# Kernel tuning notes

Measured on AMD Instinct MI355X. Metric: run time of the kernel, lower is better.

The kernel has to match this reference:

```python
import jax, jax.numpy as jnp
import numpy as np

NUM_ATOMS = 24
HID = 61          # embedding width before extended features
H = HID + 3       # conv/GRU width (degree+cycle+charge)
EMB = 64
NUM_CG = 18
NUM_ITERS = 6


def setup_inputs() -> dict:
    key = jax.random.key(0)
    ks = jax.random.split(key, 24)
    N, E = 20000, 60000
    s = 0.05
    p = lambda k, shp: (jax.random.normal(k, shp, dtype=jnp.float32) * s)
    return {
        "x": jax.random.randint(ks[0], (N, 1), 0, NUM_ATOMS),
        "edge_index": jax.random.randint(ks[1], (2, E), 0, N),
        "edge_attr": jax.random.uniform(ks[2], (E, 4), dtype=jnp.float32),
        "extended_feat": jax.random.normal(ks[3], (N, 3), dtype=jnp.float32),
        # nn.Embedding(input_dim, hidden_dim)
        "embed": p(ks[4], (NUM_ATOMS, HID)),
        # edge_nn: Linear(4,128) -> ReLU -> Linear(128, H*H)
        "We1": p(ks[5], (4, 128)), "be1": p(ks[6], (128,)),
        "We2": p(ks[7], (128, H * H)), "be2": p(ks[8], (H * H,)),
        # NNConv root weight + bias
        "root": p(ks[9], (H, H)), "conv_b": p(ks[10], (H,)),
        # GRU(H, H): torch layout [3H, H] gates order (r, z, n)
        "Wih": p(ks[11], (3 * H, H)), "Whh": p(ks[12], (3 * H, H)),
        "bih": p(ks[13], (3 * H,)), "bhh": p(ks[14], (3 * H,)),
        # output_fc: Linear(H,H) -> ReLU -> Linear(H, EMB)
        "Wo1": p(ks[15], (H, H)), "bo1": p(ks[16], (H,)),
        "Wo2": p(ks[17], (H, EMB)), "bo2": p(ks[18], (EMB,)),
        # cg_type_fc: Linear(EMB+NUM_ATOMS+3, 256) -> ReLU -> Linear(256, 18)
        "Wc1": p(ks[19], (EMB + NUM_ATOMS + 3, 256)), "bc1": p(ks[20], (256,)),
        "Wc2": p(ks[21], (256, NUM_CG)), "bc2": p(ks[22], (NUM_CG,)),
    }


def reference(x, edge_index, edge_attr, extended_feat, embed,
              We1, be1, We2, be2, root, conv_b,
              Wih, Whh, bih, bhh, Wo1, bo1, Wo2, bo2,
              Wc1, bc1, Wc2, bc2):
    N = x.shape[0]
    E = edge_index.shape[1]
    idx = x[:, 0]
    src, dst = edge_index[0], edge_index[1]

    # input_fc + relu, concat extended features -> [N, H]
    out = jax.nn.relu(embed[idx])
    out = jnp.concatenate([out, extended_feat], axis=1)
    h = out

    # edge_nn: per-edge [H, H] weight (edge_attr is constant across iterations)
    W_edge = (jax.nn.relu(edge_attr @ We1 + be1) @ We2 + be2).reshape(E, H, H)

    for _ in range(NUM_ITERS):
        # NNConv: gather source feats, per-edge matmul, scatter-add to targets
        msg = jnp.einsum('eh,ehk->ek', out[src], W_edge)          # [E, H]
        agg = jax.ops.segment_sum(msg, dst, num_segments=N)       # [N, H]
        m = jax.nn.relu(agg + out @ root + conv_b)
        # GRU cell (torch gate order r, z, n)
        gi = m @ Wih.T + bih
        gh = h @ Whh.T + bhh
        r = jax.nn.sigmoid(gi[:, :H] + gh[:, :H])
        z = jax.nn.sigmoid(gi[:, H:2 * H] + gh[:, H:2 * H])
        n = jnp.tanh(gi[:, 2 * H:] + r * gh[:, 2 * H:])
        h = (1.0 - z) * n + z * h
        out = h

    # output_fc
    out = jax.nn.relu(out @ Wo1 + bo1) @ Wo2 + bo2                # [N, EMB]

    atom_onehot = jax.nn.one_hot(idx, NUM_ATOMS, dtype=out.dtype)
    feat = jnp.concatenate([out, atom_onehot, extended_feat], axis=1)
    fg_embed = feat / jnp.maximum(
        jnp.linalg.norm(feat, axis=1, keepdims=True), 1e-12)
    node_cg_type_pred = jax.nn.relu(fg_embed @ Wc1 + bc1) @ Wc2 + bc2
    return fg_embed, node_cg_type_pred
```

## Files before the change

### kernel.cpp

```cpp
#include <hip/hip_runtime.h>
#include <hip/hip_fp16.h>

#define NATOMS 24
#define HIDD   61
#define NITERS 6
#define CTOT   132
#define HC     66

typedef unsigned short u16;
typedef unsigned int   u32;
typedef _Float16 f16x8 __attribute__((ext_vector_type(8)));
typedef float    f32x4 __attribute__((ext_vector_type(4)));

#define GLOAD_LDS16(g, l) __builtin_amdgcn_global_load_lds( \
    (const __attribute__((address_space(1))) void*)(g), \
    (__attribute__((address_space(3))) void*)(l), 16, 0, 0)

__device__ __forceinline__ float sigm(float x){ return 1.f/(1.f + __expf(-x)); }
__device__ __forceinline__ float tanhx(float x){ return 1.f - 2.f/(__expf(2.f*x)+1.f); }
__device__ __forceinline__ u16 f2h(float f){ return __half_as_ushort(__float2half(f)); }
__device__ __forceinline__ float hbits2f(u16 b){
  union { u16 u; __half h; } cv; cv.u = b; return __half2float(cv.h);
}

__device__ __forceinline__ f16x8 vmul8(f16x8 v, _Float16 s){
  f16x8 r;
  #pragma unroll
  for (int i=0;i<8;++i) r[i] = v[i]*s;
  return r;
}

__global__ void k_init_h(const int* __restrict__ x, const float* __restrict__ embed,
                         const float* __restrict__ ext, float* __restrict__ h, int N){
  int t = blockIdx.x*blockDim.x + threadIdx.x;
  if (t >= N*64) return;
  int n = t >> 6, k = t & 63;
  float v;
  if (k < HIDD) v = fmaxf(embed[x[n]*HIDD + k], 0.f);
  else          v = ext[n*3 + (k - HIDD)];
  h[t] = v;
}

__global__ void k_prep_B(const float* __restrict__ We2, const float* __restrict__ be2,
                         u16* __restrict__ Bg){
  int tid = blockIdx.x*blockDim.x + threadIdx.x;
  if (tid >= CTOT*8*64) return;
  int l  = tid & 63;
  int fi = tid >> 6;
  int ct = fi & 3;
  int kh = (fi >> 2) & 1;
  int c  = fi >> 3;
  int n  = ct*16 + (l & 15);
  int hb = kh*32 + (l >> 4)*8;
  u16 ov[8];
  #pragma unroll
  for (int j=0;j<8;++j){
    int hh = hb + j;
    float v = 0.f;
    if (c < 128)       v = We2[(size_t)c*4096 + hh*64 + n];
    else if (c == 128) v = be2[hh*64 + n];
    ov[j] = f2h(v);
  }
  uint4 o;
  o.x = (u32)ov[0] | ((u32)ov[1]<<16);
  o.y = (u32)ov[2] | ((u32)ov[3]<<16);
  o.z = (u32)ov[4] | ((u32)ov[5]<<16);
  o.w = (u32)ov[6] | ((u32)ov[7]<<16);
  *(uint4*)&Bg[(size_t)fi*512 + l*8] = o;
}

__global__ void k_prep_W(const float* __restrict__ Wo1, const float* __restrict__ Wo2,
                         const float* __restrict__ Wc1, const float* __restrict__ Wc2,
                         u16* __restrict__ Wf){
  int tid = blockIdx.x*blockDim.x + threadIdx.x;
  if (tid >= 80*64) return;
  int l  = tid & 63;
  int fi = tid >> 6;
  int lr = l & 15, lq = l >> 4;
  u16 ov[8];
  #pragma unroll
  for (int j=0;j<8;++j){
    float v = 0.f;
    if (fi < 8){
      int ct = fi >> 1, kh = fi & 1;
      int n = ct*16 + lr, k = kh*32 + lq*8 + j;
      v = Wo1[k*64 + n];
    } else if (fi < 16){
      int f2 = fi - 8;
      int ct = f2 >> 1, kh = f2 & 1;
      int n = ct*16 + lr, k = kh*32 + lq*8 + j;
      v = Wo2[k*64 + n];
    } else if (fi < 64){
      int f2 = fi - 16;
      int cti = f2 / 3, kh = f2 % 3;
      int n = cti*16 + lr, k = kh*32 + lq*8 + j;
      if (k < 91) v = Wc1[k*256 + n];
    } else {
      int f2 = fi - 64;
      int kh = f2 >> 1, ct = f2 & 1;
      int n = ct*16 + lr, k = kh*32 + lq*8 + j;
      if (n < 18) v = Wc2[k*18 + n];
    }
    ov[j] = f2h(v);
  }
  uint4 o;
  o.x = (u32)ov[0] | ((u32)ov[1]<<16);
  o.y = (u32)ov[2] | ((u32)ov[3]<<16);
  o.z = (u32)ov[4] | ((u32)ov[5]<<16);
  o.w = (u32)ov[6] | ((u32)ov[7]<<16);
  *(uint4*)&Wf[(size_t)fi*512 + l*8] = o;
}

__global__ void k_prep_C(const float* __restrict__ root, const float* __restrict__ Wih,
                         const float* __restrict__ Whh, u16* __restrict__ Cf){
  int tid = blockIdx.x*blockDim.x + threadIdx.x;
  if (tid >= 56*64) return;
  int l  = tid & 63;
  int fi = tid >> 6;
  int lr = l & 15, lq = l >> 4;
  u16 ov[8];
  #pragma unroll
  for (int j=0;j<8;++j){
    float v;
    int k = (fi < 8 ? (fi & 1) : ((fi - 8) & 1)) * 32 + lq*8 + j;
    if (fi < 8){
      int ct = fi >> 1;
      v = root[k*64 + ct*16 + lr];
    } else if (fi < 32){
      int cti = (fi - 8) >> 1;
      v = Wih[(cti*16 + lr)*64 + k];
    } else {
      int cti = (fi - 32) >> 1;
      v = Whh[(cti*16 + lr)*64 + k];
    }
    ov[j] = f2h(v);
  }
  uint4 o;
  o.x = (u32)ov[0] | ((u32)ov[1]<<16);
  o.y = (u32)ov[2] | ((u32)ov[3]<<16);
  o.z = (u32)ov[4] | ((u32)ov[5]<<16);
  o.w = (u32)ov[6] | ((u32)ov[7]<<16);
  *(uint4*)&Cf[(size_t)fi*512 + l*8] = o;
}

__global__ __launch_bounds__(256) void k_edge_mlp(
    const float* __restrict__ ea, const float* __restrict__ We1,
    const float* __restrict__ be1, u16* __restrict__ AgT, int E, int Epad)
{
  __shared__ float Al[128][66];
  int t = threadIdx.x;
  int e0 = blockIdx.x * 64;
  int el = t & 63, cg = t >> 6;
  int e = e0 + el;
  float4 av = make_float4(0,0,0,0);
  if (e < E) av = *(const float4*)&ea[(size_t)e*4];
  for (int cc = 0; cc < 32; ++cc){
    int c = cg*32 + cc;
    float v = be1[c] + av.x*We1[c] + av.y*We1[128+c] + av.z*We1[256+c] + av.w*We1[384+c];
    Al[c][el] = fmaxf(v, 0.f);
  }
  __syncthreads();
  for (int idx = t; idx < 64*33; idx += 256){
    int el2 = idx / 33, q = idx % 33;
    u16 ov[4];
    #pragma unroll
    for (int i=0;i<4;++i){
      int c = q*4 + i;
      float v;
      if (c < 128)       v = Al[c][el2];
      else if (c == 128) v = 1.f;
      else               v = 0.f;
      ov[i] = f2h(v);
    }
    ushort4 o; o.x=ov[0]; o.y=ov[1]; o.z=ov[2]; o.w=ov[3];
    *(ushort4*)&AgT[(size_t)(e0+el2)*CTOT + q*4] = o;
  }
}

__global__ __launch_bounds__(512,4) void k_msg_mfma(
    const int* __restrict__ ei, const float* __restrict__ h,
    const u16* __restrict__ AgT, const u16* __restrict__ Bg,
    float* __restrict__ agg, int E, int Epad)
{
  __shared__ __align__(16) u16 Blds[2][2][8192];
  __shared__ int dstl[128];
  int t = threadIdx.x;
  int lane = t & 63;
  int w = t >> 6;
  int eg = w & 3;
  int half = w >> 2;
  int e0 = blockIdx.x * 128;
  int slot0 = half * HC;

  if (t < 128) dstl[t] = (e0 + t < E) ? ei[E + e0 + t] : -1;

  f16x8 vf[2][2];
  #pragma unroll
  for (int rt=0; rt<2; ++rt){
    int e = e0 + eg*32 + rt*16 + (lane&15);
    int src = (e < E) ? ei[e] : 0;
    const float* hp = &h[(size_t)src*64 + (lane>>4)*8];
    #pragma unroll
    for (int kh=0; kh<2; ++kh){
      float4 a = *(const float4*)&hp[kh*32];
      float4 b = *(const float4*)&hp[kh*32+4];
      f16x8 v;
      v[0]=(_Float16)a.x; v[1]=(_Float16)a.y; v[2]=(_Float16)a.z; v[3]=(_Float16)a.w;
      v[4]=(_Float16)b.x; v[5]=(_Float16)b.y; v[6]=(_Float16)b.z; v[7]=(_Float16)b.w;
      vf[rt][kh] = v;
    }
  }

  f32x4 acc[2][4];
  #pragma unroll
  for (int i=0;i<2;++i)
    #pragma unroll
    for (int j=0;j<4;++j)
      acc[i][j] = (f32x4){0.f,0.f,0.f,0.f};

  const u16* Ae[2];
  #pragma unroll
  for (int rt=0; rt<2; ++rt)
    Ae[rt] = AgT + (size_t)(e0 + eg*32 + rt*16 + (lane&15))*CTOT + slot0;

  union UA { ushort2 u; _Float16 hv[2]; };
  _Float16 arP[2][2], arN[2][2];
  #pragma unroll
  for (int rt=0;rt<2;++rt){
    UA ua; ua.u = *(const ushort2*)&Ae[rt][0];
    arP[rt][0] = ua.hv[0]; arP[rt][1] = ua.hv[1];
  }

  {
    const char* g = (const char*)(Bg + (size_t)slot0*4096);
    #pragma unroll
    for (int r=0;r<4;++r)
      GLOAD_LDS16(g + r*4096 + eg*1024 + lane*16,
                  (char*)&Blds[half][0][0] + r*4096 + eg*1024);
  }
  __syncthreads();

  int cur = 0;
  for (int ci = 0; ci < 33; ++ci){
    if (ci + 1 < 33){
      const char* g = (const char*)(Bg + (size_t)(slot0 + (ci+1)*2)*4096);
      #pragma unroll
      for (int r=0;r<4;++r)
        GLOAD_LDS16(g + r*4096 + eg*1024 + lane*16,
                    (char*)&Blds[half][cur^1][0] + r*4096 + eg*1024);
      #pragma unroll
      for (int rt=0;rt<2;++rt){
        UA ua; ua.u = *(const ushort2*)&Ae[rt][(ci+1)*2];
        arN[rt][0] = ua.hv[0]; arN[rt][1] = ua.hv[1];
      }
    }
    const u16* Bb = &Blds[half][cur][0];
    #pragma unroll
    for (int cl=0; cl<2; ++cl){
      #pragma unroll
      for (int kh=0; kh<2; ++kh){
        f16x8 g0 = vmul8(vf[0][kh], arP[0][cl]);
        f16x8 g1 = vmul8(vf[1][kh], arP[1][cl]);
        #pragma unroll
        for (int ct=0; ct<4; ++ct){
          f16x8 bf = *(const f16x8*)&Bb[(cl*8 + kh*4 + ct)*512 + lane*8];
          acc[0][ct] = __builtin_amdgcn_mfma_f32_16x16x32_f16(g0, bf, acc[0][ct], 0,0,0);
          acc[1][ct] = __builtin_amdgcn_mfma_f32_16x16x32_f16(g1, bf, acc[1][ct], 0,0,0);
        }
      }
    }
    __syncthreads();
    #pragma unroll
    for (int rt=0;rt<2;++rt){ arP[rt][0] = arN[rt][0]; arP[rt][1] = arN[rt][1]; }
    cur ^= 1;
  }

  float* accl = (float*)&Blds[0][0][0];
  if (half == 1){
    #pragma unroll
    for (int rt=0; rt<2; ++rt)
      #pragma unroll
      for (int ct=0; ct<4; ++ct)
        *(f32x4*)&accl[(size_t)(eg*8 + rt*4 + ct)*256 + lane*4] = acc[rt][ct];
  }
  __syncthreads();
  if (half == 0){
    #pragma unroll
    for (int rt=0; rt<2; ++rt)
      #pragma unroll
      for (int ct=0; ct<4; ++ct)
        acc[rt][ct] += *(const f32x4*)&accl[(size_t)(eg*8 + rt*4 + ct)*256 + lane*4];
    #pragma unroll
    for (int rt=0; rt<2; ++rt){
      #pragma unroll
      for (int r=0; r<4; ++r){
        int el = eg*32 + rt*16 + (lane>>4)*4 + r;
        int dv = dstl[el];
        if (dv >= 0){
          #pragma unroll
          for (int ct=0; ct<4; ++ct)
            unsafeAtomicAdd(&agg[(size_t)dv*64 + ct*16 + (lane&15)], acc[rt][ct][r]);
        }
      }
    }
  }
}

__global__ __launch_bounds__(256) void k_combine(
    const float* __restrict__ hcur, float* __restrict__ agg,
    const u16* __restrict__ Cf, const float* __restrict__ convb,
    const float* __restrict__ bih, const float* __restrict__ bhh,
    float* __restrict__ hnext, int N)
{
  __shared__ __align__(16) u16  hn[32][72];
  __shared__ __align__(16) u16  mn[32][72];
  __shared__ float hsf[32][68];
  int t = threadIdx.x;
  int lane = t & 63;
  int w = t >> 6;
  int lr = lane & 15, lq = lane >> 4;
  int n0 = blockIdx.x * 32;

  {
    int node = t >> 3, k8 = (t & 7) * 8;
    int n = n0 + node;
    f16x8 v;
    float4 a = make_float4(0,0,0,0), b = make_float4(0,0,0,0);
    if (n < N){
      a = *(const float4*)&hcur[(size_t)n*64 + k8];
      b = *(const float4*)&hcur[(size_t)n*64 + k8 + 4];
    }
    v[0]=(_Float16)a.x; v[1]=(_Float16)a.y; v[2]=(_Float16)a.z; v[3]=(_Float16)a.w;
    v[4]=(_Float16)b.x; v[5]=(_Float16)b.y; v[6]=(_Float16)b.z; v[7]=(_Float16)b.w;
    *(f16x8*)&hn[node][k8] = v;
    *(float4*)&hsf[node][k8] = a;
    *(float4*)&hsf[node][k8+4] = b;
  }
  __syncthreads();

  {
    f32x4 acc[2];
    acc[0] = (f32x4){0.f,0.f,0.f,0.f}; acc[1] = (f32x4){0.f,0.f,0.f,0.f};
    #pragma unroll
    for (int kh=0; kh<2; ++kh){
      f16x8 bf = *(const f16x8*)&Cf[(size_t)(w*2 + kh)*512 + lane*8];
      #pragma unroll
      for (int rt=0; rt<2; ++rt){
        f16x8 af = *(const f16x8*)&hn[rt*16 + lr][kh*32 + lq*8];
        acc[rt] = __builtin_amdgcn_mfma_f32_16x16x32_f16(af, bf, acc[rt], 0,0,0);
      }
    }
    float cb = convb[w*16 + lr];
    #pragma unroll
    for (int rt=0; rt<2; ++rt){
      #pragma unroll
      for (int r=0; r<4; ++r){
        int node = rt*16 + lq*4 + r;
        int n = n0 + node;
        int col = w*16 + lr;
        float ag = 0.f;
        if (n < N){
          ag = agg[(size_t)n*64 + col];
          agg[(size_t)n*64 + col] = 0.f;
        }
        mn[node][col] = f2h(fmaxf(acc[rt][r] + ag + cb, 0.f));
      }
    }
  }
  __syncthreads();

  f32x4 gi[3][2], gh[3][2];
  #pragma unroll
  for (int s=0;s<3;++s)
    #pragma unroll
    for (int rt=0;rt<2;++rt){
      gi[s][rt] = (f32x4){0.f,0.f,0.f,0.f};
      gh[s][rt] = (f32x4){0.f,0.f,0.f,0.f};
    }
  #pragma unroll
  for (int s=0; s<3; ++s){
    int cti = s*4 + w;
    #pragma unroll
    for (int kh=0; kh<2; ++kh){
      f16x8 bfI = *(const f16x8*)&Cf[(size_t)(8  + cti*2 + kh)*512 + lane*8];
      f16x8 bfH = *(const f16x8*)&Cf[(size_t)(32 + cti*2 + kh)*512 + lane*8];
      #pragma unroll
      for (int rt=0; rt<2; ++rt){
        f16x8 am = *(const f16x8*)&mn[rt*16 + lr][kh*32 + lq*8];
        f16x8 ah = *(const f16x8*)&hn[rt*16 + lr][kh*32 + lq*8];
        gi[s][rt] = __builtin_amdgcn_mfma_f32_16x16x32_f16(am, bfI, gi[s][rt], 0,0,0);
        gh[s][rt] = __builtin_amdgcn_mfma_f32_16x16x32_f16(ah, bfH, gh[s][rt], 0,0,0);
      }
    }
  }

  {
    int j = w*16 + lr;
    float bI0 = bih[j], bI1 = bih[64 + j], bI2 = bih[128 + j];
    float bH0 = bhh[j], bH1 = bhh[64 + j], bH2 = bhh[128 + j];
    #pragma unroll
    for (int rt=0; rt<2; ++rt){
      #pragma unroll
      for (int r=0; r<4; ++r){
        int node = rt*16 + lq*4 + r;
        int n = n0 + node;
        if (n < N){
          float rr = sigm(gi[0][rt][r] + bI0 + gh[0][rt][r] + bH0);
          float zz = sigm(gi[1][rt][r] + bI1 + gh[1][rt][r] + bH1);
          float hold = hsf[node][j];
          float nn = tanhx(gi[2][rt][r] + bI2 + rr*(gh[2][rt][r] + bH2));
          hnext[(size_t)n*64 + j] = (1.f - zz)*nn + zz*hold;
        }
      }
    }
  }
}

__global__ __launch_bounds__(256) void k_final(
    const float* __restrict__ h, const int* __restrict__ x, const float* __restrict__ ext,
    const u16* __restrict__ Wf,
    const float* __restrict__ bo1, const float* __restrict__ bo2,
    const float* __restrict__ bc1, const float* __restrict__ bc2,
    float* __restrict__ fg_out, float* __restrict__ pred_out, int N)
{
  __shared__ __align__(16) u16 fgn[32][104];
  __shared__ __align__(16) u16 t1n[32][264];
  int t = threadIdx.x;
  int lane = t & 63;
  int w = t >> 6;
  int lr = lane & 15, lq = lane >> 4;
  int n0 = blockIdx.x * 32;

  {
    int node = t >> 3, k8 = (t & 7) * 8;
    int n = n0 + node;
    f16x8 v;
    if (n < N){
      float4 a = *(const float4*)&h[(size_t)n*64 + k8];
      float4 b = *(const float4*)&h[(size_t)n*64 + k8 + 4];
      v[0]=(_Float16)a.x; v[1]=(_Float16)a.y; v[2]=(_Float16)a.z; v[3]=(_Float16)a.w;
      v[4]=(_Float16)b.x; v[5]=(_Float16)b.y; v[6]=(_Float16)b.z; v[7]=(_Float16)b.w;
    } else {
      #pragma unroll
      for (int i=0;i<8;++i) v[i] = (_Float16)0.f;
    }
    *(f16x8*)&fgn[node][k8] = v;
    if (t < 160){
      int node2 = t / 5, qd = t % 5;
      *(uint4*)&fgn[node2][64 + qd*8] = make_uint4(0,0,0,0);
    }
  }
  __syncthreads();

  {
    f32x4 acc[2];
    acc[0] = (f32x4){0.f,0.f,0.f,0.f}; acc[1] = (f32x4){0.f,0.f,0.f,0.f};
    #pragma unroll
    for (int kh=0; kh<2; ++kh){
      f16x8 bf = *(const f16x8*)&Wf[(size_t)(w*2 + kh)*512 + lane*8];
      #pragma unroll
      for (int rt=0; rt<2; ++rt){
        f16x8 af = *(const f16x8*)&fgn[rt*16 + lr][kh*32 + lq*8];
        acc[rt] = __builtin_amdgcn_mfma_f32_16x16x32_f16(af, bf, acc[rt], 0,0,0);
      }
    }
    float bv = bo1[w*16 + lr];
    #pragma unroll
    for (int rt=0; rt<2; ++rt)
      #pragma unroll
      for (int r=0; r<4; ++r)
        t1n[rt*16 + lq*4 + r][w*16 + lr] = f2h(fmaxf(acc[rt][r] + bv, 0.f));
  }
  __syncthreads();

  {
    f32x4 acc[2];
    acc[0] = (f32x4){0.f,0.f,0.f,0.f}; acc[1] = (f32x4){0.f,0.f,0.f,0.f};
    #pragma unroll
    for (int kh=0; kh<2; ++kh){
      f16x8 bf = *(const f16x8*)&Wf[(size_t)(8 + w*2 + kh)*512 + lane*8];
      #pragma unroll
      for (int rt=0; rt<2; ++rt){
        f16x8 af = *(const f16x8*)&t1n[rt*16 + lr][kh*32 + lq*8];
        acc[rt] = __builtin_amdgcn_mfma_f32_16x16x32_f16(af, bf, acc[rt], 0,0,0);
      }
    }
    float bv = bo2[w*16 + lr];
    #pragma unroll
    for (int rt=0; rt<2; ++rt)
      #pragma unroll
      for (int r=0; r<4; ++r)
        fgn[rt*16 + lq*4 + r][w*16 + lr] = f2h(acc[rt][r] + bv);
  }
  __syncthreads();

  if (t < 32){
    int ni = t, n = n0 + ni;
    if (n < N){
      int idxn = x[n];
      float e0=ext[n*3], e1=ext[n*3+1], e2=ext[n*3+2];
      float ss = 1.f + e0*e0 + e1*e1 + e2*e2;
      for (int j=0;j<64;++j){ float v = hbits2f(fgn[ni][j]); ss += v*v; }
      float rn = 1.f / fmaxf(sqrtf(ss), 1e-12f);
      for (int j=0;j<64;++j) fgn[ni][j] = f2h(hbits2f(fgn[ni][j])*rn);
      #pragma unroll
      for (int c=0;c<24;++c) fgn[ni][64+c] = (c==idxn) ? f2h(rn) : (u16)0;
      fgn[ni][88] = f2h(e0*rn); fgn[ni][89] = f2h(e1*rn); fgn[ni][90] = f2h(e2*rn);
    }
  }
  __syncthreads();

  for (int idx=t; idx<32*91; idx+=256){
    int ni = idx / 91, c = idx % 91;
    int n = n0 + ni;
    if (n < N) fg_out[(size_t)n*91 + c] = hbits2f(fgn[ni][c]);
  }

  {
    f32x4 acc[2][4];
    #pragma unroll
    for (int i=0;i<2;++i)
      #pragma unroll
      for (int j=0;j<4;++j) acc[i][j] = (f32x4){0.f,0.f,0.f,0.f};
    #pragma unroll
    for (int kh=0; kh<3; ++kh){
      f16x8 af[2];
      #pragma unroll
      for (int rt=0; rt<2; ++rt)
        af[rt] = *(const f16x8*)&fgn[rt*16 + lr][kh*32 + lq*8];
      #pragma unroll
      for (int c4=0; c4<4; ++c4){
        int cti = w*4 + c4;
        f16x8 bf = *(const f16x8*)&Wf[(size_t)(16 + cti*3 + kh)*512 + lane*8];
        #pragma unroll
        for (int rt=0; rt<2; ++rt)
          acc[rt][c4] = __builtin_amdgcn_mfma_f32_16x16x32_f16(af[rt], bf, acc[rt][c4], 0,0,0);
      }
    }
    #pragma unroll
    for (int c4=0; c4<4; ++c4){
      float bv = bc1[w*64 + c4*16 + lr];
      #pragma unroll
      for (int rt=0; rt<2; ++rt)
        #pragma unroll
        for (int r=0; r<4; ++r)
          t1n[rt*16 + lq*4 + r][w*64 + c4*16 + lr] = f2h(fmaxf(acc[rt][c4][r] + bv, 0.f));
    }
  }
  __syncthreads();

  {
    int rt = w >> 1, ct = w & 1;
    f32x4 acc = (f32x4){0.f,0.f,0.f,0.f};
    #pragma unroll
    for (int kh=0; kh<8; ++kh){
      f16x8 af = *(const f16x8*)&t1n[rt*16 + lr][kh*32 + lq*8];
      f16x8 bf = *(const f16x8*)&Wf[(size_t)(64 + kh*2 + ct)*512 + lane*8];
      acc = __builtin_amdgcn_mfma_f32_16x16x32_f16(af, bf, acc, 0,0,0);
    }
    int c = ct*16 + lr;
    if (c < 18){
      float bv = bc2[c];
      #pragma unroll
      for (int r=0; r<4; ++r){
        int n = n0 + rt*16 + lq*4 + r;
        if (n < N) pred_out[(size_t)n*18 + c] = acc[r] + bv;
      }
    }
  }
}

extern "C" void kernel_launch(void* const* d_in, const int* in_sizes, int n_in,
                              void* d_out, int out_size, void* d_ws, size_t ws_size,
                              hipStream_t stream)
{
  const int*   x    = (const int*)d_in[0];
  const int*   ei   = (const int*)d_in[1];
  const float* ea   = (const float*)d_in[2];
  const float* ext  = (const float*)d_in[3];
  const float* embed= (const float*)d_in[4];
  const float* We1  = (const float*)d_in[5];
  const float* be1  = (const float*)d_in[6];
  const float* We2  = (const float*)d_in[7];
  const float* be2  = (const float*)d_in[8];
  const float* root = (const float*)d_in[9];
  const float* convb= (const float*)d_in[10];
  const float* Wih  = (const float*)d_in[11];
  const float* Whh  = (const float*)d_in[12];
  const float* bih  = (const float*)d_in[13];
  const float* bhh  = (const float*)d_in[14];
  const float* Wo1  = (const float*)d_in[15];
  const float* bo1  = (const float*)d_in[16];
  const float* Wo2  = (const float*)d_in[17];
  const float* bo2  = (const float*)d_in[18];
  const float* Wc1  = (const float*)d_in[19];
  const float* bc1  = (const float*)d_in[20];
  const float* Wc2  = (const float*)d_in[21];
  const float* bc2  = (const float*)d_in[22];
  int N = in_sizes[0];
  int E = in_sizes[1] / 2;
  float* out = (float*)d_out;
  float* fg_out = out;
  float* pred_out = out + (size_t)N*91;

  int nblk256 = (E + 255) / 256;
  int Epad = nblk256 * 256;
  int nblk128 = (E + 127) / 128;

  char* w = (char*)d_ws;
  size_t remain = ws_size;
  auto alloc = [&](size_t bytes)->char*{
    size_t rb = (bytes + 255) & ~(size_t)255;
    if (rb > remain) return (char*)0;
    char* p = w; w += rb; remain -= rb; return p;
  };
  float* h_a  = (float*)alloc((size_t)N*64*4);
  float* h_b  = (float*)alloc((size_t)N*64*4);
  float* agg  = (float*)alloc((size_t)N*64*4);
  u16*   AgT  = (u16*)alloc((size_t)Epad*CTOT*2);
  u16*   Bg   = (u16*)alloc((size_t)CTOT*8192);
  u16*   Wf   = (u16*)alloc((size_t)80*512*2);
  u16*   Cf   = (u16*)alloc((size_t)56*512*2);
  if (!h_a || !h_b || !agg || !AgT || !Bg || !Wf || !Cf) return;

  k_init_h<<<dim3((N*64 + 255)/256), dim3(256), 0, stream>>>(x, embed, ext, h_a, N);
  k_prep_B<<<dim3((CTOT*8*64 + 255)/256), dim3(256), 0, stream>>>(We2, be2, Bg);
  k_prep_W<<<dim3((80*64 + 255)/256), dim3(256), 0, stream>>>(Wo1, Wo2, Wc1, Wc2, Wf);
  k_prep_C<<<dim3((56*64 + 255)/256), dim3(256), 0, stream>>>(root, Wih, Whh, Cf);
  k_edge_mlp<<<dim3(Epad/64), dim3(256), 0, stream>>>(ea, We1, be1, AgT, E, Epad);
  hipMemsetAsync(agg, 0, (size_t)N*64*4, stream);

  float* hc = h_a; float* hn = h_b;
  for (int it = 0; it < NITERS; ++it){
    k_msg_mfma<<<dim3(nblk128), dim3(512), 0, stream>>>(ei, hc, AgT, Bg, agg, E, Epad);
    k_combine<<<dim3((N + 31)/32), dim3(256), 0, stream>>>(
        hc, agg, Cf, convb, bih, bhh, hn, N);
    float* tmp = hc; hc = hn; hn = tmp;
  }

  k_final<<<dim3((N + 31)/32), dim3(256), 0, stream>>>(
      hc, x, ext, Wf, bo1, bo2, bc1, bc2, fg_out, pred_out, N);
}
```

Measured before the change: 503.3 us.

## Split message kernel K-reduction across four wave groups with 1024-thread blocks

Splits the 132-slot edge-weight reduction in the message kernel over four wave quarters of 33 slots each, instead of two halves of 66, and doubles the block to 1024 threads. Each quarter streams one B slot per step into a smaller double buffer. A two-stage LDS tree reduction then combines the four partial accumulators before the atomic scatter. The aim is more parallelism per edge tile and a shorter serial loop per wave, at the cost of extra barriers, the added reduction step and heavier per-block register and LDS pressure.

```diff
diff --git a/kernel.cpp b/kernel.cpp
--- a/kernel.cpp
+++ b/kernel.cpp
@@ -5,7 +5,7 @@
 #define HIDD   61
 #define NITERS 6
 #define CTOT   132
-#define HC     66
+#define QS     33
 
 typedef unsigned short u16;
 typedef unsigned int   u32;
@@ -177,20 +177,20 @@
   }
 }
 
-__global__ __launch_bounds__(512,4) void k_msg_mfma(
+__global__ __launch_bounds__(1024,8) void k_msg_mfma(
     const int* __restrict__ ei, const float* __restrict__ h,
     const u16* __restrict__ AgT, const u16* __restrict__ Bg,
     float* __restrict__ agg, int E, int Epad)
 {
-  __shared__ __align__(16) u16 Blds[2][2][8192];
+  __shared__ __align__(16) u16 Blds[4][2][4096];
   __shared__ int dstl[128];
   int t = threadIdx.x;
   int lane = t & 63;
   int w = t >> 6;
   int eg = w & 3;
-  int half = w >> 2;
+  int q  = w >> 2;
   int e0 = blockIdx.x * 128;
-  int slot0 = half * HC;
+  int slot0 = q * QS;
 
   if (t < 128) dstl[t] = (e0 + t < E) ? ei[E + e0 + t] : -1;
 
@@ -223,73 +223,81 @@
   for (int rt=0; rt<2; ++rt)
     Ae[rt] = AgT + (size_t)(e0 + eg*32 + rt*16 + (lane&15))*CTOT + slot0;
 
-  union UA { ushort2 u; _Float16 hv[2]; };
-  _Float16 arP[2][2], arN[2][2];
-  #pragma unroll
-  for (int rt=0;rt<2;++rt){
-    UA ua; ua.u = *(const ushort2*)&Ae[rt][0];
-    arP[rt][0] = ua.hv[0]; arP[rt][1] = ua.hv[1];
-  }
+  _Float16 arP[2], arN[2];
+  #pragma unroll
+  for (int rt=0;rt<2;++rt) arP[rt] = *(const _Float16*)&Ae[rt][0];
 
   {
     const char* g = (const char*)(Bg + (size_t)slot0*4096);
     #pragma unroll
-    for (int r=0;r<4;++r)
+    for (int r=0;r<2;++r)
       GLOAD_LDS16(g + r*4096 + eg*1024 + lane*16,
-                  (char*)&Blds[half][0][0] + r*4096 + eg*1024);
+                  (char*)&Blds[q][0][0] + r*4096 + eg*1024);
   }
   __syncthreads();
 
   int cur = 0;
-  for (int ci = 0; ci < 33; ++ci){
-    if (ci + 1 < 33){
-      const char* g = (const char*)(Bg + (size_t)(slot0 + (ci+1)*2)*4096);
-      #pragma unroll
-      for (int r=0;r<4;++r)
+  for (int ci = 0; ci < QS; ++ci){
+    if (ci + 1 < QS){
+      const char* g = (const char*)(Bg + (size_t)(slot0 + ci + 1)*4096);
+      #pragma unroll
+      for (int r=0;r<2;++r)
         GLOAD_LDS16(g + r*4096 + eg*1024 + lane*16,
-                    (char*)&Blds[half][cur^1][0] + r*4096 + eg*1024);
-      #pragma unroll
-      for (int rt=0;rt<2;++rt){
-        UA ua; ua.u = *(const ushort2*)&Ae[rt][(ci+1)*2];
-        arN[rt][0] = ua.hv[0]; arN[rt][1] = ua.hv[1];
-      }
-    }
-    const u16* Bb = &Blds[half][cur][0];
-    #pragma unroll
-    for (int cl=0; cl<2; ++cl){
-      #pragma unroll
-      for (int kh=0; kh<2; ++kh){
-        f16x8 g0 = vmul8(vf[0][kh], arP[0][cl]);
-        f16x8 g1 = vmul8(vf[1][kh], arP[1][cl]);
-        #pragma unroll
-        for (int ct=0; ct<4; ++ct){
-          f16x8 bf = *(const f16x8*)&Bb[(cl*8 + kh*4 + ct)*512 + lane*8];
-          acc[0][ct] = __builtin_amdgcn_mfma_f32_16x16x32_f16(g0, bf, acc[0][ct], 0,0,0);
-          acc[1][ct] = __builtin_amdgcn_mfma_f32_16x16x32_f16(g1, bf, acc[1][ct], 0,0,0);
-        }
+                    (char*)&Blds[q][cur^1][0] + r*4096 + eg*1024);
+      #pragma unroll
+      for (int rt=0;rt<2;++rt) arN[rt] = *(const _Float16*)&Ae[rt][ci+1];
+    }
+    const u16* Bb = &Blds[q][cur][0];
+    #pragma unroll
+    for (int kh=0; kh<2; ++kh){
+      f16x8 g0 = vmul8(vf[0][kh], arP[0]);
+      f16x8 g1 = vmul8(vf[1][kh], arP[1]);
+      #pragma unroll
+      for (int ct=0; ct<4; ++ct){
+        f16x8 bf = *(const f16x8*)&Bb[(kh*4+ct)*512 + lane*8];
+        acc[0][ct] = __builtin_amdgcn_mfma_f32_16x16x32_f16(g0, bf, acc[0][ct], 0,0,0);
+        acc[1][ct] = __builtin_amdgcn_mfma_f32_16x16x32_f16(g1, bf, acc[1][ct], 0,0,0);
       }
     }
     __syncthreads();
     #pragma unroll
-    for (int rt=0;rt<2;++rt){ arP[rt][0] = arN[rt][0]; arP[rt][1] = arN[rt][1]; }
+    for (int rt=0;rt<2;++rt) arP[rt] = arN[rt];
     cur ^= 1;
   }
 
   float* accl = (float*)&Blds[0][0][0];
-  if (half == 1){
+  if (q >= 2){
+    int reg = (q-2)*4 + eg;
     #pragma unroll
     for (int rt=0; rt<2; ++rt)
       #pragma unroll
       for (int ct=0; ct<4; ++ct)
-        *(f32x4*)&accl[(size_t)(eg*8 + rt*4 + ct)*256 + lane*4] = acc[rt][ct];
-  }
-  __syncthreads();
-  if (half == 0){
+        *(f32x4*)&accl[(size_t)reg*2048 + (rt*4+ct)*256 + lane*4] = acc[rt][ct];
+  }
+  __syncthreads();
+  if (q < 2){
+    int reg = q*4 + eg;
     #pragma unroll
     for (int rt=0; rt<2; ++rt)
       #pragma unroll
       for (int ct=0; ct<4; ++ct)
-        acc[rt][ct] += *(const f32x4*)&accl[(size_t)(eg*8 + rt*4 + ct)*256 + lane*4];
+        acc[rt][ct] += *(const f32x4*)&accl[(size_t)reg*2048 + (rt*4+ct)*256 + lane*4];
+  }
+  __syncthreads();
+  if (q == 1){
+    #pragma unroll
+    for (int rt=0; rt<2; ++rt)
+      #pragma unroll
+      for (int ct=0; ct<4; ++ct)
+        *(f32x4*)&accl[(size_t)eg*2048 + (rt*4+ct)*256 + lane*4] = acc[rt][ct];
+  }
+  __syncthreads();
+  if (q == 0){
+    #pragma unroll
+    for (int rt=0; rt<2; ++rt)
+      #pragma unroll
+      for (int ct=0; ct<4; ++ct)
+        acc[rt][ct] += *(const f32x4*)&accl[(size_t)eg*2048 + (rt*4+ct)*256 + lane*4];
     #pragma unroll
     for (int rt=0; rt<2; ++rt){
       #pragma unroll
@@ -632,7 +640,7 @@
 
   float* hc = h_a; float* hn = h_b;
   for (int it = 0; it < NITERS; ++it){
-    k_msg_mfma<<<dim3(nblk128), dim3(512), 0, stream>>>(ei, hc, AgT, Bg, agg, E, Epad);
+    k_msg_mfma<<<dim3(nblk128), dim3(1024), 0, stream>>>(ei, hc, AgT, Bg, agg, E, Epad);
     k_combine<<<dim3((N + 31)/32), dim3(256), 0, stream>>>(
         hc, agg, Cf, convb, bih, bhh, hn, N);
     float* tmp = hc; hc = hn; hn = tmp;
```

Result: slower. 1.692 ms (+236.3%).
